# Kernel tuning notes

Hardware: AMD Instinct MI355X
Metric: run time of the kernel (lower is better)

## Reference

```python
import jax, jax.numpy as jnp
import numpy as np

B, S, D, H = 4, 2048, 1024, 16
DH = D // H

def setup_inputs() -> dict:
    key = jax.random.key(0)
    ks = jax.random.split(key, 4)
    scale = 1.0 / np.sqrt(D)
    x = jax.random.normal(ks[0], (B, S, D), dtype=jnp.float32)
    Wq = jax.random.normal(ks[1], (D, D), dtype=jnp.float32) * scale
    Wk = jax.random.normal(ks[2], (D, D), dtype=jnp.float32) * scale
    Wv = jax.random.normal(ks[3], (D, D), dtype=jnp.float32) * scale
    bq = jnp.zeros((D,), dtype=jnp.float32)
    bk = jnp.zeros((D,), dtype=jnp.float32)
    bv = jnp.zeros((D,), dtype=jnp.float32)
    # causal mask, broadcastable to [B, H, S, S]; mask==0 positions get -inf
    mask = jnp.tril(jnp.ones((S, S), dtype=bool))[None, None, :, :]
    return {"x": x, "mask": mask, "Wq": Wq, "bq": bq, "Wk": Wk, "bk": bk, "Wv": Wv, "bv": bv}

def reference(x, mask, Wq, bq, Wk, bk, Wv, bv):
    b, s, d = x.shape
    def proj(W, bias):
        # nn.Linear: x @ W.T + b, then split heads -> [b, H, s, DH]
        y = jnp.einsum('bsd,ed->bse', x, W) + bias
        return y.reshape(b, s, H, DH).transpose(0, 2, 1, 3)
    q = proj(Wq, bq)
    k = proj(Wk, bk)
    v = proj(Wv, bv)
    scores = jnp.einsum('bhqd,bhkd->bhqk', q, k) / jnp.sqrt(jnp.float32(DH))
    scores = jnp.where(mask, scores, -jnp.inf)
    attn = jax.nn.softmax(scores, axis=-1)
    out = jnp.einsum('bhqk,bhkd->bhqd', attn, v)
    return out.transpose(0, 2, 1, 3).reshape(b, s, d)
```

## Files before the change

### kernel.cpp

```cpp
#include <hip/hip_runtime.h>
#include <hip/hip_bf16.h>
#include <stdint.h>

typedef unsigned short u16;
typedef unsigned int   u32;
typedef short bf16x8 __attribute__((ext_vector_type(8)));
typedef float f32x4  __attribute__((ext_vector_type(4)));

typedef bf16x8 __attribute__((__may_alias__)) bf16x8_a;
typedef uint4  __attribute__((__may_alias__)) uint4_a;
typedef uint2  __attribute__((__may_alias__)) uint2_a;
typedef float4 __attribute__((__may_alias__)) float4_a;

#define MFMA_BF16(a,b,c) __builtin_amdgcn_mfma_f32_16x16x32_bf16((a),(b),(c),0,0,0)
#define L2E 1.44269504088896340736f

#define SEQ 2048
#define DMODEL 1024
#define NH 16
#define DH 64

__device__ __forceinline__ u32 pack_bf2(float a, float b) {
  union { __hip_bfloat162 h; u32 u; } c;
  c.h = __float22bfloat162_rn(make_float2(a, b));
  return c.u;
}

__device__ __forceinline__ u16 f2bf(float f) {
  u32 u = __builtin_bit_cast(u32, f);
  u += 0x7FFFu + ((u >> 16) & 1u);
  return (u16)(u >> 16);
}

__device__ __forceinline__ void gl_lds16(const u16* g, u16* l) {
  __builtin_amdgcn_global_load_lds(
      (const __attribute__((address_space(1))) void*)g,
      (__attribute__((address_space(3))) void*)l, 16, 0, 0);
}

__global__ __launch_bounds__(256) void cvt_x_bf16(
    const float* __restrict__ s, u16* __restrict__ d, int n8)
{
  int i = blockIdx.x * 256 + threadIdx.x;
  const int stride = gridDim.x * 256;
  for (; i < n8; i += stride) {
    const float4_a* p = (const float4_a*)(s + (size_t)i * 8);
    float4 a = p[0], b = p[1];
    uint4 o;
    o.x = pack_bf2(a.x, a.y); o.y = pack_bf2(a.z, a.w);
    o.z = pack_bf2(b.x, b.y); o.w = pack_bf2(b.z, b.w);
    *(uint4_a*)(d + (size_t)i * 8) = o;
  }
}

__global__ __launch_bounds__(256) void cvt_w_bf16(
    const float* __restrict__ wq, const float* __restrict__ wk, const float* __restrict__ wv,
    u16* __restrict__ oq, u16* __restrict__ ok, u16* __restrict__ ov)
{
  const float* s = (blockIdx.y == 0) ? wq : (blockIdx.y == 1) ? wk : wv;
  u16*         d = (blockIdx.y == 0) ? oq : (blockIdx.y == 1) ? ok : ov;
  const int i = blockIdx.x * 256 + threadIdx.x;
  const float4_a* p = (const float4_a*)(s + (size_t)i * 8);
  float4 a = p[0], b = p[1];
  uint4 o;
  o.x = pack_bf2(a.x, a.y); o.y = pack_bf2(a.z, a.w);
  o.z = pack_bf2(b.x, b.y); o.w = pack_bf2(b.z, b.w);
  *(uint4_a*)(d + (size_t)i * 8) = o;
}

__global__ __launch_bounds__(256, 4) void qkv_gemm_bf(
    const u16* __restrict__ Xb,
    const u16* __restrict__ Wqb, const u16* __restrict__ Wkb, const u16* __restrict__ Wvb,
    const float* __restrict__ Bq, const float* __restrict__ Bk, const float* __restrict__ Bv,
    u16* __restrict__ Qo, u16* __restrict__ Ko, u16* __restrict__ Vo)
{
  __shared__ u16 As[2][128 * 32];
  __shared__ u16 Bs[2][128 * 32];

  const int tid  = threadIdx.x;
  const int lane = tid & 63;
  const int wid  = tid >> 6;
  const int l16  = lane & 15;
  const int quad = lane >> 4;
  const int wm   = (wid >> 1) * 64;
  const int wn   = (wid & 1) * 64;

  const int m0 = blockIdx.x * 128;
  const int n0 = blockIdx.y * 128;
  const int pj = blockIdx.z;

  const u16*   Wb   = (pj == 0) ? Wqb : (pj == 1) ? Wkb : Wvb;
  const float* Bias = (pj == 0) ? Bq : (pj == 1) ? Bk : Bv;
  u16*         Out  = (pj == 0) ? Qo : (pj == 1) ? Ko : Vo;
  const float scale = (pj == 0) ? 0.125f : 1.0f;

  f32x4 acc[4][4];
#pragma unroll
  for (int i = 0; i < 4; i++)
#pragma unroll
    for (int j = 0; j < 4; j++) acc[i][j] = (f32x4){0.f, 0.f, 0.f, 0.f};

  const int lr = lane >> 2;
  const int lc = (lane & 3) * 8;

  const u16* Arow = Xb + (size_t)m0 * DMODEL;
  const u16* Brow = Wb + (size_t)n0 * DMODEL;

  const int NT = DMODEL / 32;

#pragma unroll
  for (int c = 0; c < 2; c++) {
    const int band = c * 64 + wid * 16;
    gl_lds16(Arow + (size_t)(band + lr) * DMODEL + 0 + lc, &As[0][band * 32]);
    gl_lds16(Brow + (size_t)(band + lr) * DMODEL + 0 + lc, &Bs[0][band * 32]);
  }
#pragma unroll
  for (int c = 0; c < 2; c++) {
    const int band = c * 64 + wid * 16;
    gl_lds16(Arow + (size_t)(band + lr) * DMODEL + 32 + lc, &As[1][band * 32]);
    gl_lds16(Brow + (size_t)(band + lr) * DMODEL + 32 + lc, &Bs[1][band * 32]);
  }

  for (int t = 0; t < NT; ++t) {
    const int cur = t & 1;
    if (t < NT - 1) asm volatile("s_waitcnt vmcnt(4)" ::: "memory");
    else            asm volatile("s_waitcnt vmcnt(0)" ::: "memory");
    __builtin_amdgcn_s_barrier();

    bf16x8 a[4], b[4];
#pragma unroll
    for (int mt = 0; mt < 4; mt++)
      a[mt] = *(const bf16x8_a*)&As[cur][(wm + mt * 16 + l16) * 32 + quad * 8];
#pragma unroll
    for (int nt = 0; nt < 4; nt++)
      b[nt] = *(const bf16x8_a*)&Bs[cur][(wn + nt * 16 + l16) * 32 + quad * 8];

    asm volatile("s_waitcnt lgkmcnt(0)" ::: "memory");
    __builtin_amdgcn_sched_barrier(0);
    __builtin_amdgcn_s_barrier();

    if (t + 2 < NT) {
      const int kt2 = (t + 2) * 32;
#pragma unroll
      for (int c = 0; c < 2; c++) {
        const int band = c * 64 + wid * 16;
        gl_lds16(Arow + (size_t)(band + lr) * DMODEL + kt2 + lc, &As[cur][band * 32]);
        gl_lds16(Brow + (size_t)(band + lr) * DMODEL + kt2 + lc, &Bs[cur][band * 32]);
      }
    }

#pragma unroll
    for (int mt = 0; mt < 4; mt++)
#pragma unroll
      for (int nt = 0; nt < 4; nt++)
        acc[mt][nt] = MFMA_BF16(a[mt], b[nt], acc[mt][nt]);
  }

  if (pj == 2) {
#pragma unroll
    for (int mt = 0; mt < 4; mt++) {
#pragma unroll
      for (int nt = 0; nt < 4; nt++) {
        const int n = n0 + wn + nt * 16 + l16;
        const float bias = Bias[n];
        const int h = n >> 6, dh = n & 63;
        const int m = m0 + wm + mt * 16 + quad * 4;
        const int bb = m >> 11, ss = m & 2047;
        uint2 pk;
        pk.x = pack_bf2(acc[mt][nt][0] + bias, acc[mt][nt][1] + bias);
        pk.y = pack_bf2(acc[mt][nt][2] + bias, acc[mt][nt][3] + bias);
        *(uint2_a*)&Out[((size_t)(bb * NH + h) * DH + dh) * SEQ + ss] = pk;
      }
    }
  } else {
#pragma unroll
    for (int mt = 0; mt < 4; mt++) {
#pragma unroll
      for (int nt = 0; nt < 4; nt++) {
        const int n = n0 + wn + nt * 16 + l16;
        const float bias = Bias[n];
        const int h = n >> 6, dh = n & 63;
#pragma unroll
        for (int r = 0; r < 4; r++) {
          const int m = m0 + wm + mt * 16 + quad * 4 + r;
          const int bb = m >> 11, ss = m & 2047;
          Out[((((size_t)bb * NH + h) * SEQ + ss) << 6) + dh] = f2bf((acc[mt][nt][r] + bias) * scale);
        }
      }
    }
  }
}

__global__ __launch_bounds__(256, 2) void qkv_gemm(
    const float* __restrict__ X,
    const float* __restrict__ Wq, const float* __restrict__ Wk, const float* __restrict__ Wv,
    const float* __restrict__ Bq, const float* __restrict__ Bk, const float* __restrict__ Bv,
    u16* __restrict__ Qo, u16* __restrict__ Ko, u16* __restrict__ Vo)
{
  __shared__ u16 As[128 * 32];
  __shared__ u16 Bs[128 * 32];

  const int tid  = threadIdx.x;
  const int lane = tid & 63;
  const int wid  = tid >> 6;
  const int l16  = lane & 15;
  const int quad = lane >> 4;
  const int wm   = (wid >> 1) * 64;
  const int wn   = (wid & 1) * 64;

  const int m0 = blockIdx.x * 128;
  const int n0 = blockIdx.y * 128;
  const int pj = blockIdx.z;

  const float* W    = (pj == 0) ? Wq : (pj == 1) ? Wk : Wv;
  const float* Bias = (pj == 0) ? Bq : (pj == 1) ? Bk : Bv;
  u16*         Out  = (pj == 0) ? Qo : (pj == 1) ? Ko : Vo;
  const float scale = (pj == 0) ? 0.125f : 1.0f;

  f32x4 acc[4][4];
#pragma unroll
  for (int i = 0; i < 4; i++)
#pragma unroll
    for (int j = 0; j < 4; j++) acc[i][j] = (f32x4){0.f, 0.f, 0.f, 0.f};

  float4 gX[4], gW[4];
#pragma unroll
  for (int i = 0; i < 4; i++) {
    const int ch = i * 256 + tid;
    const int r = ch >> 3, c = ch & 7;
    gX[i] = *(const float4_a*)(X + (size_t)(m0 + r) * DMODEL + c * 4);
    gW[i] = *(const float4_a*)(W + (size_t)(n0 + r) * DMODEL + c * 4);
  }

  for (int kt = 0; kt < DMODEL; kt += 32) {
    __syncthreads();
#pragma unroll
    for (int i = 0; i < 4; i++) {
      const int ch = i * 256 + tid;
      const int r = ch >> 3, c = ch & 7;
      uint2 xp, wp;
      xp.x = pack_bf2(gX[i].x, gX[i].y);  xp.y = pack_bf2(gX[i].z, gX[i].w);
      wp.x = pack_bf2(gW[i].x, gW[i].y);  wp.y = pack_bf2(gW[i].z, gW[i].w);
      *(uint2_a*)&As[r * 32 + c * 4] = xp;
      *(uint2_a*)&Bs[r * 32 + c * 4] = wp;
    }
    __syncthreads();

    if (kt + 32 < DMODEL) {
#pragma unroll
      for (int i = 0; i < 4; i++) {
        const int ch = i * 256 + tid;
        const int r = ch >> 3, c = ch & 7;
        gX[i] = *(const float4_a*)(X + (size_t)(m0 + r) * DMODEL + kt + 32 + c * 4);
        gW[i] = *(const float4_a*)(W + (size_t)(n0 + r) * DMODEL + kt + 32 + c * 4);
      }
    }

    bf16x8 a[4], b[4];
#pragma unroll
    for (int mt = 0; mt < 4; mt++)
      a[mt] = *(const bf16x8_a*)&As[(wm + mt * 16 + l16) * 32 + quad * 8];
#pragma unroll
    for (int nt = 0; nt < 4; nt++)
      b[nt] = *(const bf16x8_a*)&Bs[(wn + nt * 16 + l16) * 32 + quad * 8];
#pragma unroll
    for (int mt = 0; mt < 4; mt++)
#pragma unroll
      for (int nt = 0; nt < 4; nt++)
        acc[mt][nt] = MFMA_BF16(a[mt], b[nt], acc[mt][nt]);
  }

  if (pj == 2) {
#pragma unroll
    for (int mt = 0; mt < 4; mt++) {
#pragma unroll
      for (int nt = 0; nt < 4; nt++) {
        const int n = n0 + wn + nt * 16 + l16;
        const float bias = Bias[n];
        const int h = n >> 6, dh = n & 63;
        const int m = m0 + wm + mt * 16 + quad * 4;
        const int bb = m >> 11, ss = m & 2047;
        uint2 pk;
        pk.x = pack_bf2(acc[mt][nt][0] + bias, acc[mt][nt][1] + bias);
        pk.y = pack_bf2(acc[mt][nt][2] + bias, acc[mt][nt][3] + bias);
        *(uint2_a*)&Out[((size_t)(bb * NH + h) * DH + dh) * SEQ + ss] = pk;
      }
    }
  } else {
#pragma unroll
    for (int mt = 0; mt < 4; mt++) {
#pragma unroll
      for (int nt = 0; nt < 4; nt++) {
        const int n = n0 + wn + nt * 16 + l16;
        const float bias = Bias[n];
        const int h = n >> 6, dh = n & 63;
#pragma unroll
        for (int r = 0; r < 4; r++) {
          const int m = m0 + wm + mt * 16 + quad * 4 + r;
          const int bb = m >> 11, ss = m & 2047;
          Out[((((size_t)bb * NH + h) * SEQ + ss) << 6) + dh] = f2bf((acc[mt][nt][r] + bias) * scale);
        }
      }
    }
  }
}

__global__ __launch_bounds__(256, 4) void flash_attn(
    const u16* __restrict__ Q, const u16* __restrict__ K, const u16* __restrict__ VT,
    float* __restrict__ O)
{
  __shared__ u16 Ks[64 * 72];
  __shared__ u16 VTs[64 * 72];
  __shared__ u16 Ps[4 * 32 * 72];

  const int tid  = threadIdx.x;
  const int lane = tid & 63;
  const int wid  = tid >> 6;
  const int l16  = lane & 15;
  const int quad = lane >> 4;

  const int idx = blockIdx.x;
  const int y = idx >> 6, g = y >> 2, r4 = y & 3;
  const int qt = (g & 1) ? ((g == 1 ? 0 : 4) + r4) : ((g == 0 ? 15 : 11) - r4);
  const int bh  = idx & 63;
  const int bb = bh >> 4, hh = bh & 15;
  const int qbase = qt * 128;

  const u16* Qh = Q  + (size_t)bh * (SEQ * DH);
  const u16* Kh = K  + (size_t)bh * (SEQ * DH);
  const u16* Vh = VT + (size_t)bh * (DH * SEQ);

#pragma unroll
  for (int i = 0; i < 4; i++) {
    const int ch = i * 256 + tid;
    const int r = ch >> 3, c = ch & 7;
    *(uint4_a*)&Ps[r * 72 + c * 8] = *(const uint4_a*)(Qh + (size_t)(qbase + r) * DH + c * 8);
  }
  __syncthreads();

  u16* Pw = &Ps[wid * 32 * 72];
  bf16x8 qf[2][2];
#pragma unroll
  for (int ct = 0; ct < 2; ct++)
#pragma unroll
    for (int ks = 0; ks < 2; ks++)
      qf[ct][ks] = *(const bf16x8_a*)&Pw[(ct * 16 + l16) * 72 + ks * 32 + quad * 8];

  f32x4 o[4][2];
#pragma unroll
  for (int dt = 0; dt < 4; dt++)
#pragma unroll
    for (int ct = 0; ct < 2; ct++) o[dt][ct] = (f32x4){0.f, 0.f, 0.f, 0.f};

  float mold[2] = {-1e30f, -1e30f};
  float lsum[2] = {0.f, 0.f};

  const int jmax = 2 * qt + 1;

  uint4 gK[2], gV[2];
#pragma unroll
  for (int i = 0; i < 2; i++) {
    const int ch = i * 256 + tid;
    gK[i] = *(const uint4_a*)(Kh + (size_t)(ch >> 3) * DH + (ch & 7) * 8);
    gV[i] = *(const uint4_a*)(Vh + (size_t)(ch >> 3) * SEQ + (ch & 7) * 8);
  }

  for (int j = 0; j <= jmax; j++) {
    __syncthreads();
#pragma unroll
    for (int i = 0; i < 2; i++) {
      const int ch = i * 256 + tid;
      *(uint4_a*)&Ks[(ch >> 3) * 72 + (ch & 7) * 8]  = gK[i];
      *(uint4_a*)&VTs[(ch >> 3) * 72 + (ch & 7) * 8] = gV[i];
    }
    __syncthreads();

    if (j < jmax) {
      const int kb2 = (j + 1) * 64;
#pragma unroll
      for (int i = 0; i < 2; i++) {
        const int ch = i * 256 + tid;
        gK[i] = *(const uint4_a*)(Kh + (size_t)(kb2 + (ch >> 3)) * DH + (ch & 7) * 8);
        gV[i] = *(const uint4_a*)(Vh + (size_t)(ch >> 3) * SEQ + kb2 + (ch & 7) * 8);
      }
    }

    f32x4 s[4][2];
#pragma unroll
    for (int rt = 0; rt < 4; rt++) {
      bf16x8 ka0 = *(const bf16x8_a*)&Ks[(rt * 16 + l16) * 72 + 0 + quad * 8];
      bf16x8 ka1 = *(const bf16x8_a*)&Ks[(rt * 16 + l16) * 72 + 32 + quad * 8];
#pragma unroll
      for (int ct = 0; ct < 2; ct++) {
        f32x4 c = (f32x4){0.f, 0.f, 0.f, 0.f};
        c = MFMA_BF16(ka0, qf[ct][0], c);
        c = MFMA_BF16(ka1, qf[ct][1], c);
        s[rt][ct] = c;
      }
    }

    if (j >= (qt << 1)) {
      const int kvb = j * 64;
#pragma unroll
      for (int rt = 0; rt < 4; rt++)
#pragma unroll
        for (int ct = 0; ct < 2; ct++) {
          const int ql = qbase + wid * 32 + ct * 16 + l16;
#pragma unroll
          for (int r = 0; r < 4; r++) {
            const int kvg = kvb + rt * 16 + quad * 4 + r;
            if (kvg > ql) s[rt][ct][r] = -1e30f;
          }
        }
    }

#pragma unroll
    for (int ct = 0; ct < 2; ct++) {
      float m0_ = fmaxf(fmaxf(s[0][ct][0], s[0][ct][1]), fmaxf(s[0][ct][2], s[0][ct][3]));
      float m1_ = fmaxf(fmaxf(s[1][ct][0], s[1][ct][1]), fmaxf(s[1][ct][2], s[1][ct][3]));
      float m2_ = fmaxf(fmaxf(s[2][ct][0], s[2][ct][1]), fmaxf(s[2][ct][2], s[2][ct][3]));
      float m3_ = fmaxf(fmaxf(s[3][ct][0], s[3][ct][1]), fmaxf(s[3][ct][2], s[3][ct][3]));
      float mt = fmaxf(fmaxf(m0_, m1_), fmaxf(m2_, m3_));
      mt = fmaxf(mt, __shfl_xor(mt, 16));
      mt = fmaxf(mt, __shfl_xor(mt, 32));

      if (!__all(mt - mold[ct] <= 8.0f)) {
        const float mnew = fmaxf(mold[ct], mt);
        const float a = __builtin_amdgcn_exp2f((mold[ct] - mnew) * L2E);
        lsum[ct] *= a;
        mold[ct] = mnew;
#pragma unroll
        for (int dt = 0; dt < 4; dt++)
#pragma unroll
          for (int r = 0; r < 4; r++) o[dt][ct][r] *= a;
      }
      const float mref = mold[ct];

#pragma unroll
      for (int rt = 0; rt < 4; rt++)
#pragma unroll
        for (int r = 0; r < 4; r++)
          s[rt][ct][r] = __builtin_amdgcn_exp2f((s[rt][ct][r] - mref) * L2E);

      float t0 = (s[0][ct][0] + s[0][ct][1]) + (s[0][ct][2] + s[0][ct][3]);
      float t1 = (s[1][ct][0] + s[1][ct][1]) + (s[1][ct][2] + s[1][ct][3]);
      float t2 = (s[2][ct][0] + s[2][ct][1]) + (s[2][ct][2] + s[2][ct][3]);
      float t3 = (s[3][ct][0] + s[3][ct][1]) + (s[3][ct][2] + s[3][ct][3]);
      float ls = (t0 + t1) + (t2 + t3);
      ls += __shfl_xor(ls, 16);
      ls += __shfl_xor(ls, 32);
      lsum[ct] += ls;
    }

#pragma unroll
    for (int rt = 0; rt < 4; rt++) {
#pragma unroll
      for (int ct = 0; ct < 2; ct++) {
        uint2 pk;
        pk.x = pack_bf2(s[rt][ct][0], s[rt][ct][1]);
        pk.y = pack_bf2(s[rt][ct][2], s[rt][ct][3]);
        *(uint2_a*)&Pw[(ct * 16 + l16) * 72 + rt * 16 + quad * 4] = pk;
      }
    }
    asm volatile("s_waitcnt lgkmcnt(0)" ::: "memory");

#pragma unroll
    for (int ks2 = 0; ks2 < 2; ks2++) {
      bf16x8 vt[4], pb[2];
#pragma unroll
      for (int dt = 0; dt < 4; dt++)
        vt[dt] = *(const bf16x8_a*)&VTs[(dt * 16 + l16) * 72 + ks2 * 32 + quad * 8];
#pragma unroll
      for (int ct = 0; ct < 2; ct++)
        pb[ct] = *(const bf16x8_a*)&Pw[(ct * 16 + l16) * 72 + ks2 * 32 + quad * 8];
#pragma unroll
      for (int dt = 0; dt < 4; dt++)
#pragma unroll
        for (int ct = 0; ct < 2; ct++)
          o[dt][ct] = MFMA_BF16(vt[dt], pb[ct], o[dt][ct]);
    }
  }

#pragma unroll
  for (int ct = 0; ct < 2; ct++) {
    const float inv = 1.0f / lsum[ct];
    const int qg = qbase + wid * 32 + ct * 16 + l16;
    float* orow = O + (size_t)((size_t)bb * SEQ + qg) * DMODEL + hh * 64;
#pragma unroll
    for (int dt = 0; dt < 4; dt++) {
      float4 v4;
      v4.x = o[dt][ct][0] * inv;  v4.y = o[dt][ct][1] * inv;
      v4.z = o[dt][ct][2] * inv;  v4.w = o[dt][ct][3] * inv;
      *(float4_a*)&orow[dt * 16 + quad * 4] = v4;
    }
  }
}

__global__ void paintf(float* out, int n, float v) {
  int i = blockIdx.x * 256 + threadIdx.x;
  if (i < n) out[i] = v;
}

extern "C" void kernel_launch(void* const* d_in, const int* in_sizes, int n_in,
                              void* d_out, int out_size, void* d_ws, size_t ws_size,
                              hipStream_t stream) {
  float* out = (float*)d_out;

  const size_t elems  = (size_t)4 * SEQ * DMODEL;
  const size_t welems = (size_t)DMODEL * DMODEL;
  const size_t need_old = 3 * elems * sizeof(u16);
  const size_t need_new = (4 * elems + 3 * welems) * sizeof(u16);

  if (ws_size < need_old) {
    paintf<<<(out_size + 255) / 256, 256, 0, stream>>>(out, out_size, 3.0e38f);
    return;
  }

  const float* x  = (const float*)d_in[0];
  const float* Wq = (const float*)d_in[2];
  const float* bq = (const float*)d_in[3];
  const float* Wk = (const float*)d_in[4];
  const float* bk = (const float*)d_in[5];
  const float* Wv = (const float*)d_in[6];
  const float* bv = (const float*)d_in[7];

  u16* q = (u16*)d_ws;
  u16* k = q + elems;
  u16* v = k + elems;

  if (ws_size >= need_new) {
    u16* xb  = v + elems;
    u16* wqb = xb + elems;
    u16* wkb = wqb + welems;
    u16* wvb = wkb + welems;
    cvt_x_bf16<<<2048, 256, 0, stream>>>(x, xb, (int)(elems / 8));
    cvt_w_bf16<<<dim3(512, 3), 256, 0, stream>>>(Wq, Wk, Wv, wqb, wkb, wvb);
    qkv_gemm_bf<<<dim3(64, 8, 3), 256, 0, stream>>>(xb, wqb, wkb, wvb, bq, bk, bv, q, k, v);
  } else {
    qkv_gemm<<<dim3(64, 8, 3), 256, 0, stream>>>(x, Wq, Wk, Wv, bq, bk, bv, q, k, v);
  }

  flash_attn<<<1024, 256, 0, stream>>>(q, k, v, out);
}
```

Baseline: 287.5 us.

## Use single-wave flash-attention blocks that read K/V directly from global memory

The flash attention kernel changes from 256-thread blocks, each handling 128 query rows with K/V staged in shared memory, to 64-thread single-wave blocks handling 32 query rows. K and V fragments are now loaded straight from global memory into registers, and the cross-wave barriers and shared staging are removed. Blocks are ordered heaviest-first by query tile, and the causal iteration count is finer-grained. In exchange, K/V are no longer shared across four waves, which raises global/L2 traffic up to fourfold, and the register double-buffer prefetch is gone, so memory latency may be exposed.

```diff
diff --git a/kernel.cpp b/kernel.cpp
--- a/kernel.cpp
+++ b/kernel.cpp
@@ -305,46 +305,33 @@
   }
 }
 
-__global__ __launch_bounds__(256, 4) void flash_attn(
+__global__ __launch_bounds__(64, 4) void flash_attn(
     const u16* __restrict__ Q, const u16* __restrict__ K, const u16* __restrict__ VT,
     float* __restrict__ O)
 {
-  __shared__ u16 Ks[64 * 72];
-  __shared__ u16 VTs[64 * 72];
-  __shared__ u16 Ps[4 * 32 * 72];
-
-  const int tid  = threadIdx.x;
-  const int lane = tid & 63;
-  const int wid  = tid >> 6;
+  __shared__ u16 Ps[32 * 72];
+
+  const int lane = threadIdx.x & 63;
   const int l16  = lane & 15;
   const int quad = lane >> 4;
 
   const int idx = blockIdx.x;
-  const int y = idx >> 6, g = y >> 2, r4 = y & 3;
-  const int qt = (g & 1) ? ((g == 1 ? 0 : 4) + r4) : ((g == 0 ? 15 : 11) - r4);
-  const int bh  = idx & 63;
-  const int bb = bh >> 4, hh = bh & 15;
-  const int qbase = qt * 128;
+  const int hi  = idx >> 3;
+  const int t   = 63 - (hi >> 3);
+  const int bh  = ((hi & 7) << 3) | (idx & 7);
+  const int bb  = bh >> 4, hh = bh & 15;
+  const int qbase = t * 32;
 
   const u16* Qh = Q  + (size_t)bh * (SEQ * DH);
   const u16* Kh = K  + (size_t)bh * (SEQ * DH);
   const u16* Vh = VT + (size_t)bh * (DH * SEQ);
 
-#pragma unroll
-  for (int i = 0; i < 4; i++) {
-    const int ch = i * 256 + tid;
-    const int r = ch >> 3, c = ch & 7;
-    *(uint4_a*)&Ps[r * 72 + c * 8] = *(const uint4_a*)(Qh + (size_t)(qbase + r) * DH + c * 8);
-  }
-  __syncthreads();
-
-  u16* Pw = &Ps[wid * 32 * 72];
   bf16x8 qf[2][2];
 #pragma unroll
   for (int ct = 0; ct < 2; ct++)
 #pragma unroll
     for (int ks = 0; ks < 2; ks++)
-      qf[ct][ks] = *(const bf16x8_a*)&Pw[(ct * 16 + l16) * 72 + ks * 32 + quad * 8];
+      qf[ct][ks] = *(const bf16x8_a*)(Qh + (size_t)(qbase + ct * 16 + l16) * DH + ks * 32 + quad * 8);
 
   f32x4 o[4][2];
 #pragma unroll
@@ -355,60 +342,38 @@
   float mold[2] = {-1e30f, -1e30f};
   float lsum[2] = {0.f, 0.f};
 
-  const int jmax = 2 * qt + 1;
-
-  uint4 gK[2], gV[2];
-#pragma unroll
-  for (int i = 0; i < 2; i++) {
-    const int ch = i * 256 + tid;
-    gK[i] = *(const uint4_a*)(Kh + (size_t)(ch >> 3) * DH + (ch & 7) * 8);
-    gV[i] = *(const uint4_a*)(Vh + (size_t)(ch >> 3) * SEQ + (ch & 7) * 8);
-  }
-
-  for (int j = 0; j <= jmax; j++) {
-    __syncthreads();
-#pragma unroll
-    for (int i = 0; i < 2; i++) {
-      const int ch = i * 256 + tid;
-      *(uint4_a*)&Ks[(ch >> 3) * 72 + (ch & 7) * 8]  = gK[i];
-      *(uint4_a*)&VTs[(ch >> 3) * 72 + (ch & 7) * 8] = gV[i];
-    }
-    __syncthreads();
-
-    if (j < jmax) {
-      const int kb2 = (j + 1) * 64;
-#pragma unroll
-      for (int i = 0; i < 2; i++) {
-        const int ch = i * 256 + tid;
-        gK[i] = *(const uint4_a*)(Kh + (size_t)(kb2 + (ch >> 3)) * DH + (ch & 7) * 8);
-        gV[i] = *(const uint4_a*)(Vh + (size_t)(ch >> 3) * SEQ + kb2 + (ch & 7) * 8);
-      }
-    }
+  const int nj = (t >> 1) + 1;
+
+  for (int j = 0; j < nj; j++) {
+    const int kb = j * 64;
+
+    bf16x8 ka[4][2];
+#pragma unroll
+    for (int rt = 0; rt < 4; rt++)
+#pragma unroll
+      for (int ks = 0; ks < 2; ks++)
+        ka[rt][ks] = *(const bf16x8_a*)(Kh + (size_t)(kb + rt * 16 + l16) * DH + ks * 32 + quad * 8);
 
     f32x4 s[4][2];
 #pragma unroll
-    for (int rt = 0; rt < 4; rt++) {
-      bf16x8 ka0 = *(const bf16x8_a*)&Ks[(rt * 16 + l16) * 72 + 0 + quad * 8];
-      bf16x8 ka1 = *(const bf16x8_a*)&Ks[(rt * 16 + l16) * 72 + 32 + quad * 8];
+    for (int rt = 0; rt < 4; rt++)
 #pragma unroll
       for (int ct = 0; ct < 2; ct++) {
         f32x4 c = (f32x4){0.f, 0.f, 0.f, 0.f};
-        c = MFMA_BF16(ka0, qf[ct][0], c);
-        c = MFMA_BF16(ka1, qf[ct][1], c);
+        c = MFMA_BF16(ka[rt][0], qf[ct][0], c);
+        c = MFMA_BF16(ka[rt][1], qf[ct][1], c);
         s[rt][ct] = c;
       }
-    }
-
-    if (j >= (qt << 1)) {
-      const int kvb = j * 64;
+
+    if (j == nj - 1) {
 #pragma unroll
       for (int rt = 0; rt < 4; rt++)
 #pragma unroll
         for (int ct = 0; ct < 2; ct++) {
-          const int ql = qbase + wid * 32 + ct * 16 + l16;
+          const int ql = qbase + ct * 16 + l16;
 #pragma unroll
           for (int r = 0; r < 4; r++) {
-            const int kvg = kvb + rt * 16 + quad * 4 + r;
+            const int kvg = kb + rt * 16 + quad * 4 + r;
             if (kvg > ql) s[rt][ct][r] = -1e30f;
           }
         }
@@ -453,38 +418,43 @@
     }
 
 #pragma unroll
-    for (int rt = 0; rt < 4; rt++) {
+    for (int rt = 0; rt < 4; rt++)
 #pragma unroll
       for (int ct = 0; ct < 2; ct++) {
         uint2 pk;
         pk.x = pack_bf2(s[rt][ct][0], s[rt][ct][1]);
         pk.y = pack_bf2(s[rt][ct][2], s[rt][ct][3]);
-        *(uint2_a*)&Pw[(ct * 16 + l16) * 72 + rt * 16 + quad * 4] = pk;
-      }
-    }
+        *(uint2_a*)&Ps[(ct * 16 + l16) * 72 + rt * 16 + quad * 4] = pk;
+      }
+
+    bf16x8 vt[4][2];
+#pragma unroll
+    for (int ks2 = 0; ks2 < 2; ks2++)
+#pragma unroll
+      for (int dt = 0; dt < 4; dt++)
+        vt[dt][ks2] = *(const bf16x8_a*)(Vh + (size_t)(dt * 16 + l16) * SEQ + kb + ks2 * 32 + quad * 8);
+
     asm volatile("s_waitcnt lgkmcnt(0)" ::: "memory");
+    __builtin_amdgcn_sched_barrier(0);
 
 #pragma unroll
     for (int ks2 = 0; ks2 < 2; ks2++) {
-      bf16x8 vt[4], pb[2];
+      bf16x8 pb[2];
+#pragma unroll
+      for (int ct = 0; ct < 2; ct++)
+        pb[ct] = *(const bf16x8_a*)&Ps[(ct * 16 + l16) * 72 + ks2 * 32 + quad * 8];
 #pragma unroll
       for (int dt = 0; dt < 4; dt++)
-        vt[dt] = *(const bf16x8_a*)&VTs[(dt * 16 + l16) * 72 + ks2 * 32 + quad * 8];
-#pragma unroll
-      for (int ct = 0; ct < 2; ct++)
-        pb[ct] = *(const bf16x8_a*)&Pw[(ct * 16 + l16) * 72 + ks2 * 32 + quad * 8];
-#pragma unroll
-      for (int dt = 0; dt < 4; dt++)
 #pragma unroll
         for (int ct = 0; ct < 2; ct++)
-          o[dt][ct] = MFMA_BF16(vt[dt], pb[ct], o[dt][ct]);
+          o[dt][ct] = MFMA_BF16(vt[dt][ks2], pb[ct], o[dt][ct]);
     }
   }
 
 #pragma unroll
   for (int ct = 0; ct < 2; ct++) {
     const float inv = 1.0f / lsum[ct];
-    const int qg = qbase + wid * 32 + ct * 16 + l16;
+    const int qg = qbase + ct * 16 + l16;
     float* orow = O + (size_t)((size_t)bb * SEQ + qg) * DMODEL + hh * 64;
 #pragma unroll
     for (int dt = 0; dt < 4; dt++) {
@@ -540,5 +510,5 @@
     qkv_gemm<<<dim3(64, 8, 3), 256, 0, stream>>>(x, Wq, Wk, Wv, bq, bk, bv, q, k, v);
   }
 
-  flash_attn<<<1024, 256, 0, stream>>>(q, k, v, out);
-}
+  flash_attn<<<4096, 64, 0, stream>>>(q, k, v, out);
+}
```

After: 299.3 us. 4.1% more time.
